# Optimization experiments

Hardware: AMD Instinct MI355X
Metric: run time of the kernel (lower is better)

Reference implementation:

```python
import jax, jax.numpy as jnp
import numpy as np
import math

# Single graph (batch vector identically 0): per-graph topk and global_max_pool
# reduce to static lax.top_k and jnp.max. Pooled edge_index from SAGPooling is
# discarded because KnnEdges rebuilds the graph every layer (no_op=False).
N = 20000      # nodes
HID = 128      # in_channels == hidden_channels
L = 3          # num_layers
RATIO = 0.5    # pool_ratio
K0, KINC = 6, 2  # KnnEdges start_k / k_increment
OUT = 5


def setup_inputs() -> dict:
    key = jax.random.key(0)
    ks = jax.random.split(key, 10)
    s = 0.05  # keep tanh scores unsaturated
    x = jax.random.normal(ks[0], (N, HID), jnp.float32)
    pos = jax.random.uniform(ks[1], (N, 2), jnp.float32) * 100.0
    src = jax.random.randint(ks[2], (N * K0,), 0, N)
    dst = jnp.repeat(jnp.arange(N), K0)
    edge_index = jnp.stack([src, dst]).astype(jnp.int32)  # [2, E], row0=src(j), row1=dst(i)
    return dict(
        x=x, pos=pos, edge_index=edge_index,
        Wrel=jax.random.normal(ks[3], (L, HID, HID), jnp.float32) * s,
        brel=jnp.zeros((L, HID), jnp.float32),
        Wroot=jax.random.normal(ks[4], (L, HID, HID), jnp.float32) * s,
        Wprel=jax.random.normal(ks[5], (L, HID), jnp.float32) * s,
        bprel=jnp.zeros((L,), jnp.float32),
        Wproot=jax.random.normal(ks[6], (L, HID), jnp.float32) * s,
        W1=jax.random.normal(ks[7], (HID * L, HID), jnp.float32) * s,
        b1=jnp.zeros((HID,), jnp.float32),
        W2=jax.random.normal(ks[8], (HID, OUT), jnp.float32) * s,
        b2=jnp.zeros((OUT,), jnp.float32),
    )


def _mean_agg(x, src, dst, n):
    # mean over incoming messages x_j for each target i (PyG aggr='mean'; 0 if isolated)
    ssum = jax.ops.segment_sum(x[src], dst, num_segments=n)
    deg = jax.ops.segment_sum(jnp.ones(src.shape, x.dtype), dst, num_segments=n)
    return ssum / jnp.maximum(deg, 1.0)[:, None]


def reference(x, pos, edge_index, Wrel, brel, Wroot, Wprel, bprel, Wproot, W1, b1, W2, b2):
    src, dst = edge_index[0], edge_index[1]
    n = x.shape[0]
    xs = []
    for i in range(L):
        # GraphConv(aggr='mean'): out_i = W_rel @ mean_j x_j + W_root @ x_i + b
        agg = _mean_agg(x, src, dst, n)
        x = jax.nn.relu(agg @ Wrel[i] + x @ Wroot[i] + brel[i])
        # SAGPooling: score GNN = GraphConv(hid->1, aggr='add'); tanh nonlinearity
        sagg = jax.ops.segment_sum(x[src], dst, num_segments=n)
        score = jnp.tanh(sagg @ Wprel[i] + x @ Wproot[i] + bprel[i])  # [n]
        k_keep = math.ceil(RATIO * n)
        vals, perm = jax.lax.top_k(score, k_keep)
        x = x[perm] * vals[:, None]
        xs.append(jnp.max(x, axis=0))  # global_max_pool (single graph)
        # KnnEdges: pos = pos[perm]; rebuild KNN graph with k = start_k + i*k_increment
        pos = pos[perm]
        n = k_keep
        k = K0 + KINC * i
        d2 = jnp.sum((pos[:, None, :] - pos[None, :, :]) ** 2, axis=-1)  # [n, n]
        d2 = jnp.where(jnp.eye(n, dtype=bool), jnp.inf, d2)  # loop=False
        _, nbr = jax.lax.top_k(-d2, k)  # [n, k] nearest neighbors
        src = nbr.reshape(-1)                 # neighbor j (source)
        dst = jnp.repeat(jnp.arange(n), k)    # query i (target)
    h = jnp.concatenate(xs)  # JumpingKnowledge mode='cat' -> [HID*L]
    h = jax.nn.relu(h @ W1 + b1)  # dropout p=0.5 in eval mode: identity
    return (h @ W2 + b2)[None, :]  # [1, OUT]
```

## Files before the change

### kernel.cpp

```cpp
#include <hip/hip_runtime.h>
#include <hip/hip_bf16.h>
#include <math.h>

#define HID 128
#define PR 20
#define CRPB 32
#define CAND_CAP 8192
#define MAXEQ 8192
#define MAXCELLS 4096

__device__ inline int wave_iscan(int v, int lane) {
#pragma unroll
  for (int off = 1; off < 64; off <<= 1) {
    int o = __shfl_up(v, off, 64);
    if (lane >= off) v += o;
  }
  return v;
}

template <int K>
__global__ __launch_bounds__(256) void k_conv_fused(
    const float* __restrict__ x, const int* __restrict__ src, int n, float invk,
    const float* __restrict__ Wrel, const float* __restrict__ Wroot,
    const float* __restrict__ brel,
    const float* __restrict__ wprel, const float* __restrict__ wproot,
    float* __restrict__ out, float* __restrict__ uo, float* __restrict__ vo) {
  __shared__ float4 sagg4[CRPB][HID / 4];
  __shared__ float4 sx4[CRPB][HID / 4];
  __shared__ int ssrc[CRPB * K];
  int t = threadIdx.x;
  int i0 = blockIdx.x * CRPB;
  const int nK = n * K;
  for (int s = t; s < CRPB * K; s += 256) {
    int gi = i0 * K + s;
    int v = (gi < nK) ? src[gi] : 0;
    ssrc[s] = ((unsigned)v < (unsigned)n) ? v : 0;
  }
  __syncthreads();
  {
    int fq = t & 31, h = t >> 5;
    const float4* x4 = (const float4*)x;
    for (int r = h; r < CRPB; r += 8) {
      int row = i0 + r;
      float4 s = make_float4(0.f, 0.f, 0.f, 0.f);
      float4 xv = make_float4(0.f, 0.f, 0.f, 0.f);
      if (row < n) {
#pragma unroll
        for (int j = 0; j < K; ++j) {
          float4 xx = x4[(size_t)ssrc[r * K + j] * 32 + fq];
          s.x += xx.x; s.y += xx.y; s.z += xx.z; s.w += xx.w;
        }
        xv = x4[(size_t)row * 32 + fq];
      }
      s.x *= invk; s.y *= invk; s.z *= invk; s.w *= invk;
      sagg4[r][fq] = s;
      sx4[r][fq] = xv;
    }
  }
  __syncthreads();
  int q = t & 31, rg = t >> 5;
  const float4* Wrel4  = (const float4*)Wrel;
  const float4* Wroot4 = (const float4*)Wroot;
  float4 bq = ((const float4*)brel)[q];
  float4 acc[4];
#pragma unroll
  for (int rr = 0; rr < 4; ++rr) acc[rr] = bq;
  int rbase = rg * 4;
#pragma unroll 2
  for (int cq = 0; cq < HID / 4; ++cq) {
    float4 w1[4], w2[4];
#pragma unroll
    for (int uu = 0; uu < 4; ++uu) {
      w1[uu] = Wrel4[(cq * 4 + uu) * 32 + q];
      w2[uu] = Wroot4[(cq * 4 + uu) * 32 + q];
    }
#pragma unroll
    for (int rr = 0; rr < 4; ++rr) {
      float4 a  = sagg4[rbase + rr][cq];
      float4 xx = sx4[rbase + rr][cq];
      acc[rr].x += a.x*w1[0].x + a.y*w1[1].x + a.z*w1[2].x + a.w*w1[3].x
                 + xx.x*w2[0].x + xx.y*w2[1].x + xx.z*w2[2].x + xx.w*w2[3].x;
      acc[rr].y += a.x*w1[0].y + a.y*w1[1].y + a.z*w1[2].y + a.w*w1[3].y
                 + xx.x*w2[0].y + xx.y*w2[1].y + xx.z*w2[2].y + xx.w*w2[3].y;
      acc[rr].z += a.x*w1[0].z + a.y*w1[1].z + a.z*w1[2].z + a.w*w1[3].z
                 + xx.x*w2[0].z + xx.y*w2[1].z + xx.z*w2[2].z + xx.w*w2[3].z;
      acc[rr].w += a.x*w1[0].w + a.y*w1[1].w + a.z*w1[2].w + a.w*w1[3].w
                 + xx.x*w2[0].w + xx.y*w2[1].w + xx.z*w2[2].w + xx.w*w2[3].w;
    }
  }
  float4 wplq = ((const float4*)wprel)[q];
  float4 wprq = ((const float4*)wproot)[q];
#pragma unroll
  for (int rr = 0; rr < 4; ++rr) {
    int row = i0 + rbase + rr;
    float4 v = acc[rr];
    v.x = v.x > 0.f ? v.x : 0.f;
    v.y = v.y > 0.f ? v.y : 0.f;
    v.z = v.z > 0.f ? v.z : 0.f;
    v.w = v.w > 0.f ? v.w : 0.f;
    float pu = 0.f, pv = 0.f;
    if (row < n) {
      ((float4*)out)[(size_t)row * 32 + q] = v;
      pu = v.x * wplq.x + v.y * wplq.y + v.z * wplq.z + v.w * wplq.w;
      pv = v.x * wprq.x + v.y * wprq.y + v.z * wprq.z + v.w * wprq.w;
    }
#pragma unroll
    for (int o = 16; o; o >>= 1) {
      pu += __shfl_down(pu, o, 32);
      pv += __shfl_down(pv, o, 32);
    }
    if (q == 0 && row < n) { uo[row] = pu; vo[row] = pv; }
  }
}

template <int K>
__global__ void k_score_lite(const float* __restrict__ u, const float* __restrict__ v,
                             const int* __restrict__ src, const float* __restrict__ bprel,
                             int n, float* __restrict__ score, unsigned* __restrict__ key) {
  int i = blockIdx.x * blockDim.x + threadIdx.x;
  if (i >= n) return;
  float s = v[i] + bprel[0];
#pragma unroll
  for (int j = 0; j < K; ++j) s += u[src[i * K + j]];
  float sc = tanhf(s);
  score[i] = sc;
  unsigned bb = __float_as_uint(sc);
  key[i] = (bb & 0x80000000u) ? ~bb : (bb | 0x80000000u);
}

__global__ __launch_bounds__(128) void k_hist(const unsigned* __restrict__ key, int n4,
                                              unsigned* __restrict__ ghist) {
  __shared__ unsigned lh[1024];
  int t = threadIdx.x;
#pragma unroll
  for (int u = 0; u < 8; ++u) lh[t + u * 128] = 0u;
  __syncthreads();
  int i = blockIdx.x * 128 + t;
  if (i < n4) {
    uint4 kv = ((const uint4*)key)[i];
    atomicAdd(&lh[kv.x >> 22], 1u);
    atomicAdd(&lh[kv.y >> 22], 1u);
    atomicAdd(&lh[kv.z >> 22], 1u);
    atomicAdd(&lh[kv.w >> 22], 1u);
  }
  __syncthreads();
#pragma unroll
  for (int u = 0; u < 8; ++u) {
    unsigned v = lh[t + u * 128];
    if (v) atomicAdd(&ghist[t + u * 128], v);
  }
}

__global__ __launch_bounds__(1024) void k_pickbin(const unsigned* __restrict__ ghist, int kk,
                                                  unsigned* __restrict__ BA) {
  __shared__ int wtA[16];
  __shared__ unsigned sh_B, sh_above;
  int t = threadIdx.x;
  int lane = t & 63, wid = t >> 6;
  unsigned hv = ghist[t];
  int iv = wave_iscan((int)hv, lane);
  if (lane == 63) wtA[wid] = iv;
  __syncthreads();
  int b = 0, tot = 0;
#pragma unroll
  for (int w2 = 0; w2 < 16; ++w2) { int s = wtA[w2]; if (w2 < wid) b += s; tot += s; }
  unsigned val = (unsigned)(iv + b);
  unsigned above_strict = (unsigned)tot - val;
  unsigned above_incl = above_strict + hv;
  if (above_incl >= (unsigned)kk && above_strict < (unsigned)kk) {
    sh_B = (unsigned)t;
    sh_above = above_strict;
  }
  __syncthreads();
  if (t == 0) { BA[0] = sh_B; BA[1] = sh_above; }
}

__global__ void k_collect(const unsigned* __restrict__ key, int n,
                          const unsigned* __restrict__ BA,
                          unsigned* __restrict__ candbuf, int* __restrict__ candCnt) {
  int i = blockIdx.x * blockDim.x + threadIdx.x;
  int lane = threadIdx.x & 63;
  unsigned long long lmask = (1ull << lane) - 1ull;
  unsigned B = BA[0];
  unsigned kv = (i < n) ? key[i] : 0u;
  bool m = (i < n) && ((kv >> 22) == B);
  unsigned long long mm = __ballot(m);
  if (mm) {
    int leader = (int)(__ffsll((long long)mm) - 1);
    int base = 0;
    if (lane == leader) base = atomicAdd(candCnt, (int)__popcll(mm));
    base = __shfl(base, leader, 64);
    if (m) {
      int p = base + (int)__popcll(mm & lmask);
      if (p < CAND_CAP) candbuf[p] = kv;
    }
  }
}

__global__ __launch_bounds__(1024) void k_refine(const unsigned* __restrict__ candbuf,
                                                 const int* __restrict__ candCnt,
                                                 const unsigned* __restrict__ BA, int kk,
                                                 unsigned* __restrict__ outTG) {
  __shared__ unsigned cand[CAND_CAP];
  __shared__ unsigned hist256[256];
  __shared__ unsigned sh_remain, sh_prefix;
  __shared__ int wtB[4];
  int t = threadIdx.x;
  int lane = t & 63, wid = t >> 6;
  unsigned B = BA[0], above = BA[1];
  int remain = kk - (int)above;
  int cnt = *candCnt; if (cnt > CAND_CAP) cnt = CAND_CAP;
  for (int i = t; i < cnt; i += 1024) cand[i] = candbuf[i];
  if (t == 0) { sh_prefix = 0u; sh_remain = (unsigned)remain; }
  __syncthreads();
  for (int pass = 0; pass < 4; ++pass) {
    int shift = 24 - pass * 8;
    unsigned prefix = sh_prefix;
    unsigned rem = sh_remain;
    if (t < 256) hist256[t] = 0u;
    __syncthreads();
    unsigned himask = (pass == 0) ? 0u : (0xFFFFFFFFu << (shift + 8));
    for (int i = t; i < cnt; i += 1024) {
      unsigned kky = cand[i];
      if ((kky & himask) == prefix) atomicAdd(&hist256[(kky >> shift) & 255u], 1u);
    }
    __syncthreads();
    int hv = (t < 256) ? (int)hist256[t] : 0;
    int iv = wave_iscan(hv, lane);
    if (t < 256 && lane == 63) wtB[wid] = iv;
    __syncthreads();
    if (t < 256) {
      int b = 0, tot = 0;
#pragma unroll
      for (int w2 = 0; w2 < 4; ++w2) { int s = wtB[w2]; if (w2 < wid) b += s; tot += s; }
      unsigned val = (unsigned)(iv + b);
      unsigned sstrict = (unsigned)tot - val;
      if (sstrict < rem && sstrict + (unsigned)hv >= rem) {
        sh_prefix = prefix | ((unsigned)t << shift);
        sh_remain = rem - sstrict;
      }
    }
    __syncthreads();
  }
  if (t == 0) {
    outTG[0] = sh_prefix;
    outTG[1] = above + (unsigned)remain - sh_remain;
  }
}

__global__ void k_sel(const unsigned* __restrict__ key, int n,
                      const unsigned* __restrict__ TG,
                      int* __restrict__ perm, int* __restrict__ cntGt,
                      int* __restrict__ eqbuf, int* __restrict__ cntEq) {
  int i = blockIdx.x * blockDim.x + threadIdx.x;
  int lane = threadIdx.x & 63;
  unsigned long long lmask = (1ull << lane) - 1ull;
  unsigned T = TG[0];
  unsigned kv = (i < n) ? key[i] : 0u;
  bool g = (i < n) && (kv > T);
  bool e = (i < n) && (kv == T);
  unsigned long long mg = __ballot(g);
  unsigned long long me = __ballot(e);
  if (mg) {
    int leader = (int)(__ffsll((long long)mg) - 1);
    int base = 0;
    if (lane == leader) base = atomicAdd(cntGt, (int)__popcll(mg));
    base = __shfl(base, leader, 64);
    if (g) perm[base + (int)__popcll(mg & lmask)] = i;
  }
  if (me) {
    int leader = (int)(__ffsll((long long)me) - 1);
    int base = 0;
    if (lane == leader) base = atomicAdd(cntEq, (int)__popcll(me));
    base = __shfl(base, leader, 64);
    if (e) {
      int p = base + (int)__popcll(me & lmask);
      if (p < MAXEQ) eqbuf[p] = i;
    }
  }
}

__global__ void k_sel_eq_fin(const unsigned* __restrict__ TG, const int* __restrict__ eqbuf,
                             const int* __restrict__ cntEq, int* __restrict__ perm, int kk) {
  int lane = threadIdx.x;
  int G = (int)TG[1];
  int need = kk - G;
  int cnt = *cntEq; if (cnt > MAXEQ) cnt = MAXEQ;
  int prev = -1;
  for (int t = 0; t < need; ++t) {
    int mymin = 0x7fffffff;
    for (int u = lane; u < cnt; u += 64) {
      int v = eqbuf[u];
      if (v > prev && v < mymin) mymin = v;
    }
    for (int o = 1; o < 64; o <<= 1) mymin = min(mymin, __shfl_xor(mymin, o, 64));
    if (lane == 0) perm[G + t] = mymin;
    prev = mymin;
  }
}

template <int R>
__global__ __launch_bounds__(256) void k_pool_pmax(
    const float* __restrict__ x, const float* __restrict__ score,
    const int* __restrict__ perm, const float* __restrict__ pos_in,
    float* __restrict__ xout, float* __restrict__ pos_out, int store,
    float* __restrict__ pmax, int* __restrict__ counts, int Gg, float inv_w) {
  __shared__ float sm[2][HID];
  int f = threadIdx.x & 127;
  int half = threadIdx.x >> 7;
  int j0 = blockIdx.x * R;
  float mx = -1e30f;
  for (int r = half; r < R; r += 2) {
    int j = j0 + r;
    int node = perm[j];
    float v = score[node];
    float val = x[(size_t)node * HID + f] * v;
    if (store) {
      xout[(size_t)j * HID + f] = val;
      if (f == 0) {
        float px = pos_in[node * 2], py = pos_in[node * 2 + 1];
        pos_out[j * 2] = px; pos_out[j * 2 + 1] = py;
        int cx = min(Gg - 1, max(0, (int)(px * inv_w)));
        int cy = min(Gg - 1, max(0, (int)(py * inv_w)));
        atomicAdd(&counts[cy * Gg + cx], 1);
      }
    }
    mx = fmaxf(mx, val);
  }
  sm[half][f] = mx;
  __syncthreads();
  if (half == 0) pmax[blockIdx.x * HID + f] = fmaxf(sm[0][f], sm[1][f]);
}

__global__ __launch_bounds__(1024) void k_grid_scan(const int* __restrict__ counts,
                                                    int* __restrict__ starts,
                                                    int* __restrict__ cursor, int cells) {
  __shared__ int wtA[16];
  int t = threadIdx.x;
  int lane = t & 63, wid = t >> 6;
  int c0[4]; int base4 = t * 4; int s = 0;
#pragma unroll
  for (int u = 0; u < 4; ++u) {
    int idx = base4 + u;
    c0[u] = (idx < cells) ? counts[idx] : 0;
    s += c0[u];
  }
  int is = wave_iscan(s, lane);
  if (lane == 63) wtA[wid] = is;
  __syncthreads();
  int b = 0;
#pragma unroll
  for (int w2 = 0; w2 < 16; ++w2) { if (w2 < wid) b += wtA[w2]; }
  int excl = b + is - s;
#pragma unroll
  for (int u = 0; u < 4; ++u) {
    int idx = base4 + u;
    if (idx < cells) { starts[idx] = excl; cursor[idx] = excl; excl += c0[u]; }
  }
}

__global__ void k_grid_scatter(const float2* __restrict__ pos, int m, int Gg, float inv_w,
                               int* __restrict__ cursor, float2* __restrict__ spos,
                               int* __restrict__ sidx) {
  int i = blockIdx.x * blockDim.x + threadIdx.x;
  if (i >= m) return;
  float2 p = pos[i];
  int cx = min(Gg - 1, max(0, (int)(p.x * inv_w)));
  int cy = min(Gg - 1, max(0, (int)(p.y * inv_w)));
  int pp = atomicAdd(&cursor[cy * Gg + cx], 1);
  spos[pp] = p;
  sidx[pp] = i;
}

template <int K>
__global__ __launch_bounds__(256) void k_knn_wave(const float2* __restrict__ spos,
                           const int* __restrict__ sidx,
                           const int* __restrict__ starts, const int* __restrict__ counts,
                           int m, int G, float w, float inv_w, int* __restrict__ src_out) {
  int lane = threadIdx.x & 63;
  int j = blockIdx.x * (blockDim.x >> 6) + (threadIdx.x >> 6);
  if (j >= m) return;
  float2 qp = spos[j];
  int q = sidx[j];
  int cx = min(G - 1, max(0, (int)(qp.x * inv_w)));
  int cy = min(G - 1, max(0, (int)(qp.y * inv_w)));

  float bd[K]; int bi[K];
#pragma unroll
  for (int t = 0; t < K; ++t) { bd[t] = 1e30f; bi[t] = 0; }

  auto scan_span = [&](int s, int e) {
    for (int p = s + lane; p < e; p += 64) {
      if (p == j) continue;
      float2 pp = spos[p];
      float dx = qp.x - pp.x, dy = qp.y - pp.y;
      float d = dx * dx + dy * dy;
      if (d < bd[K - 1]) {
        float dd = d; int ii = sidx[p];
#pragma unroll
        for (int t = 0; t < K; ++t) {
          bool sw = dd < bd[t];
          float od = bd[t]; int oi = bi[t];
          if (sw) { bd[t] = dd; bi[t] = ii; dd = od; ii = oi; }
        }
      }
    }
  };

  {
    int xl = max(0, cx - 1), xh = min(G - 1, cx + 1);
    int y0 = max(0, cy - 1), y1 = min(G - 1, cy + 1);
    int ss[3], ee[3]; int nr = 0;
    for (int y = y0; y <= y1; ++y) {
      int b = y * G;
      ss[nr] = starts[b + xl];
      ee[nr] = starts[b + xh] + counts[b + xh];
      ++nr;
    }
    for (int t = 0; t < nr; ++t) scan_span(ss[t], ee[t]);
  }

  int r = 1;
  unsigned long long mg[K];
  while (true) {
    unsigned long long tmp[K];
#pragma unroll
    for (int t = 0; t < K; ++t)
      tmp[t] = ((unsigned long long)__float_as_uint(bd[t]) << 32) | (unsigned)bi[t];
#pragma unroll
    for (int t = 0; t < K; ++t) {
      unsigned long long mn = tmp[0];
#pragma unroll
      for (int o = 1; o < 64; o <<= 1) {
        unsigned long long ot = __shfl_xor(mn, o, 64);
        if (ot < mn) mn = ot;
      }
      mg[t] = mn;
      if (tmp[0] == mn) {
#pragma unroll
        for (int s2 = 0; s2 < K - 1; ++s2) tmp[s2] = tmp[s2 + 1];
        tmp[K - 1] = ~0ull;
      }
    }
    float kth = __uint_as_float((unsigned)(mg[K - 1] >> 32));
    float bnd = 1e30f;
    if (cx - r > 0)     bnd = fminf(bnd, qp.x - (float)(cx - r) * w);
    if (cx + r < G - 1) bnd = fminf(bnd, (float)(cx + r + 1) * w - qp.x);
    if (cy - r > 0)     bnd = fminf(bnd, qp.y - (float)(cy - r) * w);
    if (cy + r < G - 1) bnd = fminf(bnd, (float)(cy + r + 1) * w - qp.y);
    if (bnd > 1e29f) break;
    float bb = fmaxf(bnd, 0.f) * 0.999f;
    if (kth < bb * bb) break;
    ++r;
    int xl = max(0, cx - r), xh = min(G - 1, cx + r);
    int yt = cy - r, yb = cy + r;
    if (yt >= 0)     { int b = yt * G; scan_span(starts[b + xl], starts[b + xh] + counts[b + xh]); }
    if (yb <= G - 1) { int b = yb * G; scan_span(starts[b + xl], starts[b + xh] + counts[b + xh]); }
    int ylo = max(0, cy - r + 1), yhi = min(G - 1, cy + r - 1);
    for (int y = ylo; y <= yhi; ++y) {
      int b = y * G;
      if (cx - r >= 0)     { int c = b + cx - r; scan_span(starts[c], starts[c] + counts[c]); }
      if (cx + r <= G - 1) { int c = b + cx + r; scan_span(starts[c], starts[c] + counts[c]); }
    }
  }
  if (lane == 0) {
#pragma unroll
    for (int t = 0; t < K; ++t) src_out[q * K + t] = (int)(unsigned)(mg[t] & 0xffffffffu);
  }
}

__global__ __launch_bounds__(256) void k_colmax2(const float* __restrict__ pmax,
                                                 int P0, int P1, int P2,
                                                 float* __restrict__ pmax2) {
  __shared__ float sm[2][HID];
  int l = blockIdx.x >> 3, c = blockIdx.x & 7;
  int lo3[3] = {0, P0, P0 + P1};
  int len3[3] = {P0, P1, P2};
  int lo = lo3[l], len = len3[l];
  int f = threadIdx.x & 127, half = threadIdx.x >> 7;
  float mx = -1e30f;
  for (int p = c + 8 * half; p < len; p += 16)
    mx = fmaxf(mx, pmax[(size_t)(lo + p) * HID + f]);
  sm[half][f] = mx;
  __syncthreads();
  if (half == 0) pmax2[(size_t)blockIdx.x * HID + f] = fmaxf(sm[0][f], sm[1][f]);
}

__global__ __launch_bounds__(1024) void k_final(const float* __restrict__ pmax2,
                        const float* __restrict__ W1, const float* __restrict__ b1,
                        const float* __restrict__ W2, const float* __restrict__ b2,
                        float* __restrict__ out) {
  __shared__ float sxs[3 * HID];
  __shared__ float red[8][HID];
  __shared__ float h1[HID];
  int f = threadIdx.x & 127, ch = threadIdx.x >> 7;
  if (ch < 3) {
    float mx = pmax2[(size_t)(ch * 8) * HID + f];
#pragma unroll
    for (int u = 1; u < 8; ++u) mx = fmaxf(mx, pmax2[(size_t)(ch * 8 + u) * HID + f]);
    sxs[ch * HID + f] = mx;
  }
  __syncthreads();
  float acc = 0.f;
  for (int c = ch * 48; c < (ch + 1) * 48; ++c) acc += sxs[c] * W1[c * HID + f];
  red[ch][f] = acc;
  __syncthreads();
  if (ch == 0) {
    float a = b1[f];
#pragma unroll
    for (int u = 0; u < 8; ++u) a += red[u][f];
    h1[f] = a > 0.f ? a : 0.f;
  }
  __syncthreads();
  if (threadIdx.x < 5) {
    float a = b2[threadIdx.x];
    for (int c = 0; c < HID; ++c) a += h1[c] * W2[c * 5 + threadIdx.x];
    out[threadIdx.x] = a;
  }
}

extern "C" void kernel_launch(void* const* d_in, const int* in_sizes, int n_in,
                              void* d_out, int out_size, void* d_ws, size_t ws_size,
                              hipStream_t stream) {
  const float* x_in   = (const float*)d_in[0];
  const float* pos_in = (const float*)d_in[1];
  const int*   ei     = (const int*)d_in[2];
  const float* Wrel   = (const float*)d_in[3];
  const float* brel   = (const float*)d_in[4];
  const float* Wroot  = (const float*)d_in[5];
  const float* Wprel  = (const float*)d_in[6];
  const float* bprel  = (const float*)d_in[7];
  const float* Wproot = (const float*)d_in[8];
  const float* W1     = (const float*)d_in[9];
  const float* b1     = (const float*)d_in[10];
  const float* W2     = (const float*)d_in[11];
  const float* b2     = (const float*)d_in[12];
  float* out = (float*)d_out;

  const int N0 = in_sizes[0] / HID;
  const int P0 = (N0 / 2) / PR, P1 = (N0 / 4) / PR, P2 = (N0 / 8) / PR;

  char* w = (char*)d_ws;
  float*    xB     = (float*)w;    w += (size_t)N0 * HID * 4;
  float*    xA     = (float*)w;    w += (size_t)(N0 / 2) * HID * 4;
  float*    score  = (float*)w;    w += (size_t)N0 * 4;
  unsigned* key    = (unsigned*)w; w += (size_t)N0 * 4;
  float*    ubuf   = (float*)w;    w += (size_t)N0 * 4;
  float*    vbuf   = (float*)w;    w += (size_t)N0 * 4;
  float*    posA   = (float*)w;    w += (size_t)(N0 / 2) * 2 * 4;
  float*    posB   = (float*)w;    w += (size_t)(N0 / 2) * 2 * 4;
  int*      srcbuf = (int*)w;      w += (size_t)(N0 / 2) * 8 * 4;
  int*      permb  = (int*)w;      w += (size_t)(N0 / 2) * 4;
  float*    pmax   = (float*)w;    w += (size_t)(P0 + P1 + P2) * HID * 4;
  float*    pmax2  = (float*)w;    w += (size_t)24 * HID * 4;
  unsigned* ghist  = (unsigned*)w; w += 1024 * 4;
  int*      cnt    = (int*)w;      w += 32;
  int*      counts = (int*)w;      w += MAXCELLS * 4;
  const size_t ZERO_BYTES = 1024 * 4 + 32 + MAXCELLS * 4;
  unsigned* TG     = (unsigned*)w; w += 16;
  unsigned* BA     = (unsigned*)w; w += 16;
  unsigned* candbuf= (unsigned*)w; w += CAND_CAP * 4;
  int*      eqbuf  = (int*)w;      w += MAXEQ * 4;
  int*      starts = (int*)w;      w += MAXCELLS * 4;
  int*      cursor = (int*)w;      w += MAXCELLS * 4;
  float2*   spos   = (float2*)w;   w += (size_t)(N0 / 2) * 8;
  int*      sidx   = (int*)w;      w += (size_t)(N0 / 2) * 4;
  (void)ws_size; (void)n_in; (void)out_size;

  int n = N0;
  const float* xcur   = x_in;
  const float* poscur = pos_in;
  const int*   srccur = ei;
  int kcur = 6;
  int Poff = 0;

  for (int l = 0; l < 3; ++l) {
    const int kk = n / 2;
    int Gg = (int)ceilf(sqrtf((float)kk / 2.5f));
    if (Gg > 64) Gg = 64;
    if (Gg < 1) Gg = 1;
    int cells = Gg * Gg;
    float cw = 100.f / (float)Gg;
    float inv_w = (float)Gg / 100.f;
    int cblocks = (n + CRPB - 1) / CRPB;

    hipMemsetAsync(ghist, 0, ZERO_BYTES, stream);

    if (kcur == 6) {
      k_conv_fused<6><<<cblocks, 256, 0, stream>>>(xcur, srccur, n, 1.f / 6.f,
          Wrel + l * HID * HID, Wroot + l * HID * HID, brel + l * HID,
          Wprel + l * HID, Wproot + l * HID, xB, ubuf, vbuf);
      k_score_lite<6><<<(n + 255) / 256, 256, 0, stream>>>(ubuf, vbuf, srccur, bprel + l,
                                                           n, score, key);
    } else {
      k_conv_fused<8><<<cblocks, 256, 0, stream>>>(xcur, srccur, n, 1.f / 8.f,
          Wrel + l * HID * HID, Wroot + l * HID * HID, brel + l * HID,
          Wprel + l * HID, Wproot + l * HID, xB, ubuf, vbuf);
      k_score_lite<8><<<(n + 255) / 256, 256, 0, stream>>>(ubuf, vbuf, srccur, bprel + l,
                                                           n, score, key);
    }
    int n4 = n >> 2;
    k_hist<<<(n4 + 127) / 128, 128, 0, stream>>>(key, n4, ghist);
    k_pickbin<<<1, 1024, 0, stream>>>(ghist, kk, BA);
    k_collect<<<(n + 255) / 256, 256, 0, stream>>>(key, n, BA, candbuf, cnt + 2);
    k_refine<<<1, 1024, 0, stream>>>(candbuf, cnt + 2, BA, kk, TG);
    k_sel<<<(n + 255) / 256, 256, 0, stream>>>(key, n, TG, permb, cnt, eqbuf, cnt + 1);
    k_sel_eq_fin<<<1, 64, 0, stream>>>(TG, eqbuf, cnt + 1, permb, kk);

    float* pos_out = (l == 0) ? posA : posB;
    int store = (l < 2) ? 1 : 0;
    k_pool_pmax<PR><<<kk / PR, 256, 0, stream>>>(xB, score, permb, poscur, xA, pos_out,
                                                 store, pmax + (size_t)Poff * HID,
                                                 counts, Gg, inv_w);
    Poff += kk / PR;
    n = kk;
    if (l < 2) {
      k_grid_scan<<<1, 1024, 0, stream>>>(counts, starts, cursor, cells);
      k_grid_scatter<<<(n + 255) / 256, 256, 0, stream>>>((const float2*)pos_out, n, Gg, inv_w,
                                                          cursor, spos, sidx);
      if (l == 0) { k_knn_wave<6><<<(n + 3) / 4, 256, 0, stream>>>(spos, sidx, starts, counts,
                                                                   n, Gg, cw, inv_w, srcbuf); kcur = 6; }
      else        { k_knn_wave<8><<<(n + 3) / 4, 256, 0, stream>>>(spos, sidx, starts, counts,
                                                                   n, Gg, cw, inv_w, srcbuf); kcur = 8; }
    }
    xcur = xA; poscur = pos_out; srccur = srcbuf;
  }
  k_colmax2<<<24, 256, 0, stream>>>(pmax, P0, P1, P2, pmax2);
  k_final<<<1, 1024, 0, stream>>>(pmax2, W1, b1, W2, b2, out);
}
```

Before: 266.4 us.

## Fuse histogram into score kernel and bin pick into collect, hoist memset

The coarse radix histogram is now built inside the score kernel, so the separate histogram pass is gone. Every collect block redundantly scans the 1024-bin histogram to find the pivot bin, which removes the single-block pickbin launch. Per-layer histogram, counter and grid-count buffers are allocated separately so one memset before the loop replaces the per-layer memsets. The cost is redundant scan work in each collect block and more shared-memory atomics in the score kernel.

```diff
diff --git a/kernel.cpp b/kernel.cpp
--- a/kernel.cpp
+++ b/kernel.cpp
@@ -114,74 +114,69 @@
 }
 
 template <int K>
-__global__ void k_score_lite(const float* __restrict__ u, const float* __restrict__ v,
-                             const int* __restrict__ src, const float* __restrict__ bprel,
-                             int n, float* __restrict__ score, unsigned* __restrict__ key) {
-  int i = blockIdx.x * blockDim.x + threadIdx.x;
-  if (i >= n) return;
-  float s = v[i] + bprel[0];
-#pragma unroll
-  for (int j = 0; j < K; ++j) s += u[src[i * K + j]];
-  float sc = tanhf(s);
-  score[i] = sc;
-  unsigned bb = __float_as_uint(sc);
-  key[i] = (bb & 0x80000000u) ? ~bb : (bb | 0x80000000u);
-}
-
-__global__ __launch_bounds__(128) void k_hist(const unsigned* __restrict__ key, int n4,
-                                              unsigned* __restrict__ ghist) {
+__global__ __launch_bounds__(256) void k_score_lite(
+    const float* __restrict__ u, const float* __restrict__ v,
+    const int* __restrict__ src, const float* __restrict__ bprel,
+    int n, float* __restrict__ score, unsigned* __restrict__ key,
+    unsigned* __restrict__ ghist) {
   __shared__ unsigned lh[1024];
   int t = threadIdx.x;
 #pragma unroll
-  for (int u = 0; u < 8; ++u) lh[t + u * 128] = 0u;
-  __syncthreads();
-  int i = blockIdx.x * 128 + t;
-  if (i < n4) {
-    uint4 kv = ((const uint4*)key)[i];
-    atomicAdd(&lh[kv.x >> 22], 1u);
-    atomicAdd(&lh[kv.y >> 22], 1u);
-    atomicAdd(&lh[kv.z >> 22], 1u);
-    atomicAdd(&lh[kv.w >> 22], 1u);
-  }
-  __syncthreads();
-#pragma unroll
-  for (int u = 0; u < 8; ++u) {
-    unsigned v = lh[t + u * 128];
-    if (v) atomicAdd(&ghist[t + u * 128], v);
-  }
-}
-
-__global__ __launch_bounds__(1024) void k_pickbin(const unsigned* __restrict__ ghist, int kk,
-                                                  unsigned* __restrict__ BA) {
-  __shared__ int wtA[16];
-  __shared__ unsigned sh_B, sh_above;
+  for (int uu = 0; uu < 4; ++uu) lh[t + uu * 256] = 0u;
+  __syncthreads();
+  int i = blockIdx.x * 256 + t;
+  if (i < n) {
+    float s = v[i] + bprel[0];
+#pragma unroll
+    for (int j = 0; j < K; ++j) s += u[src[i * K + j]];
+    float sc = tanhf(s);
+    score[i] = sc;
+    unsigned bb = __float_as_uint(sc);
+    unsigned k2 = (bb & 0x80000000u) ? ~bb : (bb | 0x80000000u);
+    key[i] = k2;
+    atomicAdd(&lh[k2 >> 22], 1u);
+  }
+  __syncthreads();
+#pragma unroll
+  for (int uu = 0; uu < 4; ++uu) {
+    unsigned vv = lh[t + uu * 256];
+    if (vv) atomicAdd(&ghist[t + uu * 256], vv);
+  }
+}
+
+__global__ __launch_bounds__(256) void k_collect(
+    const unsigned* __restrict__ key, int n, int kk,
+    const unsigned* __restrict__ ghist,
+    unsigned* __restrict__ BA, unsigned* __restrict__ candbuf, int* __restrict__ candCnt) {
+  __shared__ int wt[4];
+  __shared__ unsigned shB, shAbove;
   int t = threadIdx.x;
   int lane = t & 63, wid = t >> 6;
-  unsigned hv = ghist[t];
-  int iv = wave_iscan((int)hv, lane);
-  if (lane == 63) wtA[wid] = iv;
+  unsigned h[4]; int s = 0;
+#pragma unroll
+  for (int uu = 0; uu < 4; ++uu) { h[uu] = ghist[t * 4 + uu]; s += (int)h[uu]; }
+  int is = wave_iscan(s, lane);
+  if (lane == 63) wt[wid] = is;
   __syncthreads();
   int b = 0, tot = 0;
 #pragma unroll
-  for (int w2 = 0; w2 < 16; ++w2) { int s = wtA[w2]; if (w2 < wid) b += s; tot += s; }
-  unsigned val = (unsigned)(iv + b);
-  unsigned above_strict = (unsigned)tot - val;
-  unsigned above_incl = above_strict + hv;
-  if (above_incl >= (unsigned)kk && above_strict < (unsigned)kk) {
-    sh_B = (unsigned)t;
-    sh_above = above_strict;
-  }
-  __syncthreads();
-  if (t == 0) { BA[0] = sh_B; BA[1] = sh_above; }
-}
-
-__global__ void k_collect(const unsigned* __restrict__ key, int n,
-                          const unsigned* __restrict__ BA,
-                          unsigned* __restrict__ candbuf, int* __restrict__ candCnt) {
-  int i = blockIdx.x * blockDim.x + threadIdx.x;
-  int lane = threadIdx.x & 63;
+  for (int w2 = 0; w2 < 4; ++w2) { int ss = wt[w2]; if (w2 < wid) b += ss; tot += ss; }
+  int c = b + is - s;
+#pragma unroll
+  for (int uu = 0; uu < 4; ++uu) {
+    c += (int)h[uu];
+    unsigned above_strict = (unsigned)(tot - c);
+    unsigned above_incl = above_strict + h[uu];
+    if (above_incl >= (unsigned)kk && above_strict < (unsigned)kk) {
+      shB = (unsigned)(t * 4 + uu);
+      shAbove = above_strict;
+    }
+  }
+  __syncthreads();
+  unsigned B = shB;
+  if (blockIdx.x == 0 && t == 0) { BA[0] = B; BA[1] = shAbove; }
+  int i = blockIdx.x * 256 + t;
   unsigned long long lmask = (1ull << lane) - 1ull;
-  unsigned B = BA[0];
   unsigned kv = (i < n) ? key[i] : 0u;
   bool m = (i < n) && ((kv >> 22) == B);
   unsigned long long mm = __ballot(m);
@@ -207,7 +202,7 @@
   __shared__ int wtB[4];
   int t = threadIdx.x;
   int lane = t & 63, wid = t >> 6;
-  unsigned B = BA[0], above = BA[1];
+  unsigned above = BA[1];
   int remain = kk - (int)above;
   int cnt = *candCnt; if (cnt > CAND_CAP) cnt = CAND_CAP;
   for (int i = t; i < cnt; i += 1024) cand[i] = candbuf[i];
@@ -553,10 +548,10 @@
   int*      permb  = (int*)w;      w += (size_t)(N0 / 2) * 4;
   float*    pmax   = (float*)w;    w += (size_t)(P0 + P1 + P2) * HID * 4;
   float*    pmax2  = (float*)w;    w += (size_t)24 * HID * 4;
-  unsigned* ghist  = (unsigned*)w; w += 1024 * 4;
-  int*      cnt    = (int*)w;      w += 32;
-  int*      counts = (int*)w;      w += MAXCELLS * 4;
-  const size_t ZERO_BYTES = 1024 * 4 + 32 + MAXCELLS * 4;
+  unsigned* ghistB = (unsigned*)w; w += 3 * 1024 * 4;
+  int*      cnt    = (int*)w;      w += 16 * 4;
+  int*      countsB= (int*)w;      w += 2 * MAXCELLS * 4;
+  const size_t ZERO_BYTES = 3 * 1024 * 4 + 16 * 4 + 2 * MAXCELLS * 4;
   unsigned* TG     = (unsigned*)w; w += 16;
   unsigned* BA     = (unsigned*)w; w += 16;
   unsigned* candbuf= (unsigned*)w; w += CAND_CAP * 4;
@@ -567,6 +562,8 @@
   int*      sidx   = (int*)w;      w += (size_t)(N0 / 2) * 4;
   (void)ws_size; (void)n_in; (void)out_size;
 
+  hipMemsetAsync(ghistB, 0, ZERO_BYTES, stream);
+
   int n = N0;
   const float* xcur   = x_in;
   const float* poscur = pos_in;
@@ -583,29 +580,26 @@
     float cw = 100.f / (float)Gg;
     float inv_w = (float)Gg / 100.f;
     int cblocks = (n + CRPB - 1) / CRPB;
-
-    hipMemsetAsync(ghist, 0, ZERO_BYTES, stream);
+    unsigned* ghist = ghistB + l * 1024;
+    int* counts = countsB + (l < 2 ? l : 0) * MAXCELLS;
 
     if (kcur == 6) {
       k_conv_fused<6><<<cblocks, 256, 0, stream>>>(xcur, srccur, n, 1.f / 6.f,
           Wrel + l * HID * HID, Wroot + l * HID * HID, brel + l * HID,
           Wprel + l * HID, Wproot + l * HID, xB, ubuf, vbuf);
       k_score_lite<6><<<(n + 255) / 256, 256, 0, stream>>>(ubuf, vbuf, srccur, bprel + l,
-                                                           n, score, key);
+                                                           n, score, key, ghist);
     } else {
       k_conv_fused<8><<<cblocks, 256, 0, stream>>>(xcur, srccur, n, 1.f / 8.f,
           Wrel + l * HID * HID, Wroot + l * HID * HID, brel + l * HID,
           Wprel + l * HID, Wproot + l * HID, xB, ubuf, vbuf);
       k_score_lite<8><<<(n + 255) / 256, 256, 0, stream>>>(ubuf, vbuf, srccur, bprel + l,
-                                                           n, score, key);
-    }
-    int n4 = n >> 2;
-    k_hist<<<(n4 + 127) / 128, 128, 0, stream>>>(key, n4, ghist);
-    k_pickbin<<<1, 1024, 0, stream>>>(ghist, kk, BA);
-    k_collect<<<(n + 255) / 256, 256, 0, stream>>>(key, n, BA, candbuf, cnt + 2);
-    k_refine<<<1, 1024, 0, stream>>>(candbuf, cnt + 2, BA, kk, TG);
-    k_sel<<<(n + 255) / 256, 256, 0, stream>>>(key, n, TG, permb, cnt, eqbuf, cnt + 1);
-    k_sel_eq_fin<<<1, 64, 0, stream>>>(TG, eqbuf, cnt + 1, permb, kk);
+                                                           n, score, key, ghist);
+    }
+    k_collect<<<(n + 255) / 256, 256, 0, stream>>>(key, n, kk, ghist, BA, candbuf, cnt + 3 * l + 2);
+    k_refine<<<1, 1024, 0, stream>>>(candbuf, cnt + 3 * l + 2, BA, kk, TG);
+    k_sel<<<(n + 255) / 256, 256, 0, stream>>>(key, n, TG, permb, cnt + 3 * l, eqbuf, cnt + 3 * l + 1);
+    k_sel_eq_fin<<<1, 64, 0, stream>>>(TG, eqbuf, cnt + 3 * l + 1, permb, kk);
 
     float* pos_out = (l == 0) ? posA : posB;
     int store = (l < 2) ? 1 : 0;
```

Measured after the change: 253.0 us. 1.05x faster.
